# Optimization experiments

Measured on AMD Instinct MI355X. Metric: run time of the kernel, lower is better.

## Reference

```python
import jax, jax.numpy as jnp
import numpy as np

B, N = 512, 128          # molecules, max atoms
T = 10                   # NLSQ gradient-descent steps
STEP_EPS = 0.1
ALPHA, ALPHA_BASE = 5.0, 0.1
K_RANK, POWER_STEPS = 3, 10


def setup_inputs() -> dict:
    key = jax.random.key(0)
    k1, k2, k3, k4 = jax.random.split(key, 4)
    edge_pred = jax.random.normal(k1, (B, N, N, 2), dtype=jnp.float32)
    a = jax.random.randint(k2, (B, N, N), 0, 2)
    adj = ((a + a.transpose(0, 2, 1)) > 0).astype(jnp.int32)
    adj = adj * (1 - jnp.eye(N, dtype=jnp.int32))[None]  # symmetric, zero diagonal
    d_init = jnp.full((1,), 4.0, dtype=jnp.float32)      # learned scalar param
    u_init = jax.random.normal(k3, (B, N, 3), dtype=jnp.float32)   # power-iter inits (k=3 cols)
    x_noise = jax.random.normal(k4, (B, N, 3), dtype=jnp.float32)  # x_init additive noise
    return {"edge_pred": edge_pred, "adj": adj, "d_init": d_init,
            "u_init": u_init, "x_noise": x_noise}


def distances(X):
    # X: [B,N,3] -> [B,N,N]
    diff = X[:, None, :, :] - X[:, :, None, :]
    return jnp.sqrt(jnp.sum(diff * diff, axis=-1) + 0.01)


def distance_to_gram(D, mask):
    N_mol = jnp.sum(mask, axis=1)[:, 0].reshape(-1, 1, 1)
    D2 = D * D
    D_row = jnp.sum(D2, axis=1, keepdims=True) / N_mol
    D_col = jnp.sum(D2, axis=2, keepdims=True) / N_mol
    D_mean = jnp.sum(D2, axis=(1, 2), keepdims=True) / (N_mol * N_mol)
    return mask * (-0.5) * (D2 - D_row - D_col + D_mean)


def low_rank_approx_power(A, u_init):
    # A: [B,N,N]; u_init: [B,N,K_RANK] -> X: [B,N,K_RANK]
    A_lr = A
    cols = []
    for kx in range(K_RANK):
        u = u_init[..., kx:kx + 1]  # [B,N,1]
        for _ in range(POWER_STEPS):
            norm = jnp.sqrt(jnp.sum(u * u, axis=1, keepdims=True))
            u = u / jnp.maximum(norm, 1e-3)  # F.normalize(dim=1, eps=1e-3)
            u = jnp.matmul(A_lr, u)
        eig_sq = jnp.sum(u * u, axis=1, keepdims=True)
        u = u / jnp.power(eig_sq + 0.01, 0.25)
        cols.append(u)
        A_lr = A_lr - jnp.matmul(u, u.transpose(0, 2, 1))
    return jnp.concatenate(cols, axis=2)


def dist_nlsq(D, W, mask, u_init, x_noise):
    def objective(X):
        D_X = distances(X)
        U = jnp.sum(mask * W * jnp.square(D - D_X), axis=(1, 2)) / jnp.sum(mask, axis=(1, 2))
        return jnp.sum(U)

    gradfun = jax.grad(objective)
    Bg = distance_to_gram(D, mask)
    x0 = low_rank_approx_power(Bg, u_init) + x_noise

    def step(x, t):
        g = gradfun(x)
        dx = -STEP_EPS * g
        speed = jnp.sqrt(jnp.sum(dx * dx, axis=2, keepdims=True) + 0.001)
        alpha_t = ALPHA_BASE + (ALPHA - ALPHA_BASE) * ((T - t) / T)
        scale = alpha_t * jnp.tanh(speed / alpha_t) / speed
        return x + dx * scale, None

    x, _ = jax.lax.scan(step, x0, jnp.arange(T, dtype=jnp.float32))
    return x


def reference(edge_pred, adj, d_init, u_init, x_noise):
    diag_mask = adj.astype(jnp.float32)                      # [B,N,N], zero diagonal
    ep = edge_pred + edge_pred.transpose(0, 2, 1, 3)         # symmetrize
    preds = jax.nn.softplus(d_init + ep) * diag_mask[..., None]
    D, W = preds[..., 0], preds[..., 1]
    eye = jnp.eye(N, dtype=bool)[None]
    mask = jnp.where(eye, 1.0, diag_mask)                    # diagonal set to 1
    X = dist_nlsq(D, W, mask, u_init, x_noise)               # [B,N,3]
    return diag_mask * distances(X)
```

## Files before the change

### kernel.cpp

```cpp
#include <hip/hip_runtime.h>
#include <hip/hip_fp16.h>
#include <math.h>

#define NN   128
#define PSTR 132
#define NTH  512

__device__ __forceinline__ float sp_softplus(float x) {
    float p = __builtin_amdgcn_exp2f(fabsf(x) * -1.44269504f);
    float l = __builtin_amdgcn_logf(1.0f + p);
    return fmaxf(x, 0.0f) + 0.69314718f * l;
}
__device__ __forceinline__ float rdlane(float v, int l) {
    return __int_as_float(__builtin_amdgcn_readlane(__float_as_int(v), l));
}
__device__ __forceinline__ float rcpf(float x)  { return __builtin_amdgcn_rcpf(x); }
__device__ __forceinline__ float rsqf(float x)  { return __builtin_amdgcn_rsqf(x); }

__global__ void __launch_bounds__(NTH, 2)
ts_gcn_kernel(const float* __restrict__ edge_pred,
              const int*   __restrict__ adj,
              const float* __restrict__ d_init,
              const float* __restrict__ u_init,
              const float* __restrict__ x_noise,
              float* __restrict__ out)
{
    __shared__ __align__(16) float pool[NN * PSTR];
    __shared__ unsigned maskb[512];
    __shared__ int s_cntM, s_cntN0;

    float* scrA = pool;
    float* scrB = pool + 512;
    float* scrC = pool + 1024;
    float* Xx   = pool + 1536;
    float* Xy   = pool + 1664;
    float* Xz   = pool + 1792;
    float* r_s  = pool + 1920;

    const int b    = blockIdx.x;
    const int t    = threadIdx.x;
    const int lane = t & 63;
    const int i    = t & 127;
    const int q    = t >> 7;
    const int jb   = q * 32;
    const int lsel = jb & 63;
    const int hi6  = (t >> 6) & 1;

    const float dini = d_init[0];
    if (t == 0) { s_cntM = 0; s_cntN0 = 0; }

    const int4* adj4 = (const int4*)(adj + (size_t)b * 16384);
    #pragma unroll 4
    for (int k = 0; k < 8; ++k) {
        int e4 = t + k * 512;
        int4 v = adj4[e4];
        int ii = e4 >> 5, jj = (e4 & 31) * 4;
        float* p = &pool[ii * PSTR + jj];
        p[0] = __int_as_float(v.x); p[1] = __int_as_float(v.y);
        p[2] = __int_as_float(v.z); p[3] = __int_as_float(v.w);
    }
    __syncthreads();
    unsigned mword = 0;
    #pragma unroll
    for (int k = 0; k < 32; ++k) {
        int j = jb + k;
        int a = __float_as_int(pool[i * PSTR + j]) | __float_as_int(pool[j * PSTR + i]);
        if (a != 0 && i != j) mword |= (1u << k);
    }
    maskb[i * 4 + q] = mword;
    int cm = __popc(mword);
    #pragma unroll
    for (int off = 32; off; off >>= 1) cm += __shfl_xor(cm, off);
    if (lane == 0) atomicAdd(&s_cntM, cm);
    if (i == 0)    atomicAdd(&s_cntN0, __popc(mword));
    __syncthreads();

    const float4* ep4 = (const float4*)(edge_pred + (size_t)b * 32768);
    #pragma unroll 4
    for (int k = 0; k < 16; ++k) {
        int e2 = t + k * 512;
        float4 v = ep4[e2];
        int ii = e2 >> 6, jj = (e2 & 63) * 2;
        *(float2*)&pool[ii * PSTR + jj] = make_float2(v.x, v.z);
    }
    __syncthreads();
    float    Dfull[32];
    unsigned DWh[32];
    #pragma unroll
    for (int k = 0; k < 32; ++k) {
        int j = jb + k;
        float s = pool[i * PSTR + j] + pool[j * PSTR + i];
        float d = ((mword >> k) & 1) ? sp_softplus(dini + s) : 0.f;
        Dfull[k] = d;
        DWh[k] = (unsigned)__half_as_ushort(__float2half_rn(d));
    }
    __syncthreads();

    float rp = 0.f;
    #pragma unroll
    for (int k = 0; k < 32; ++k) rp = fmaf(Dfull[k], Dfull[k], rp);
    scrA[t] = rp;
    __syncthreads();
    if (t < NN)
        r_s[t] = (scrA[t] + scrA[t + 128]) + (scrA[t + 256] + scrA[t + 384]);
    __syncthreads();
    float mt = r_s[lane] + r_s[lane + 64];
    #pragma unroll
    for (int off = 32; off; off >>= 1) mt += __shfl_xor(mt, off);

    const float Nmol  = (float)(1 + s_cntN0);
    const float Minv  = 1.0f / (float)(128 + s_cntM);
    const float invN  = 1.0f / Nmol;
    const float cmean = mt * invN * invN;

    const float ri = r_s[i];
    float Bg[32];
    #pragma unroll
    for (int k = 0; k < 32; ++k) {
        int j = jb + k;
        float dv = Dfull[k];
        float v  = -0.5f * (dv * dv - ri * invN - r_s[j] * invN + cmean);
        bool msk = ((mword >> k) & 1) || (i == j);
        Bg[k] = msk ? v : 0.f;
    }
    __syncthreads();

    #pragma unroll 4
    for (int k = 0; k < 16; ++k) {
        int e2 = t + k * 512;
        float4 v = ep4[e2];
        int ii = e2 >> 6, jj = (e2 & 63) * 2;
        *(float2*)&pool[ii * PSTR + jj] = make_float2(v.y, v.w);
    }
    __syncthreads();
    #pragma unroll
    for (int k = 0; k < 32; ++k) {
        int j = jb + k;
        float s = pool[i * PSTR + j] + pool[j * PSTR + i];
        float w = ((mword >> k) & 1) ? sp_softplus(dini + s) : 0.f;
        DWh[k] |= ((unsigned)__half_as_ushort(__float2half_rn(w))) << 16;
    }
    __syncthreads();

    const float* ub = u_init  + (size_t)b * 384;
    const float* xb = x_noise + (size_t)b * 384;

    #pragma unroll 1
    for (int kx = 0; kx < 3; ++kx) {
        float ulo = ub[lane * 3 + kx];
        float uhi = ub[(lane + 64) * 3 + kx];
        float* rd = scrA; float* wr = scrB;
        #pragma unroll 1
        for (int s = 0; s < 10; ++s) {
            if (s) {
                ulo = (rd[lane]      + rd[lane + 128]) + (rd[lane + 256] + rd[lane + 384]);
                uhi = (rd[lane + 64] + rd[lane + 192]) + (rd[lane + 320] + rd[lane + 448]);
            }
            float n2 = fmaf(ulo, ulo, uhi * uhi);
            #pragma unroll
            for (int off = 32; off; off >>= 1) n2 += __shfl_xor(n2, off);
            float inv = rcpf(fmaxf(sqrtf(n2), 0.001f));
            float usel = (q < 2) ? ulo : uhi;
            float a0 = 0.f, a1 = 0.f;
            #pragma unroll
            for (int k = 0; k < 16; ++k) {
                a0 = fmaf(Bg[k],      rdlane(usel, lsel + k),      a0);
                a1 = fmaf(Bg[k + 16], rdlane(usel, lsel + k + 16), a1);
            }
            wr[t] = (a0 + a1) * inv;
            __syncthreads();
            float* tmp = rd; rd = wr; wr = tmp;
        }
        float ulo2 = (rd[lane]      + rd[lane + 128]) + (rd[lane + 256] + rd[lane + 384]);
        float uhi2 = (rd[lane + 64] + rd[lane + 192]) + (rd[lane + 320] + rd[lane + 448]);
        float e2 = fmaf(ulo2, ulo2, uhi2 * uhi2);
        #pragma unroll
        for (int off = 32; off; off >>= 1) e2 += __shfl_xor(e2, off);
        float esc  = rsqf(sqrtf(e2 + 0.01f));
        float ufi  = (hi6 ? uhi2 : ulo2) * esc;
        float uscl = ((q < 2) ? ulo2 : uhi2) * esc;
        #pragma unroll
        for (int k = 0; k < 32; ++k)
            Bg[k] = fmaf(-ufi, rdlane(uscl, lsel + k), Bg[k]);
        if (t < NN) {
            float* Xc = (kx == 0) ? Xx : (kx == 1) ? Xy : Xz;
            Xc[t] = ufi + xb[t * 3 + kx];
        }
        __syncthreads();
    }

    const float stepc = 0.4f * Minv;
    #pragma unroll 1
    for (int st = 0; st < 10; ++st) {
        float xix = Xx[i], xiy = Xy[i], xiz = Xz[i];
        float gx = 0.f, gy = 0.f, gz = 0.f;
        #pragma unroll
        for (int g = 0; g < 8; ++g) {
            float4 vx = *(const float4*)&Xx[jb + 4 * g];
            float4 vy = *(const float4*)&Xy[jb + 4 * g];
            float4 vz = *(const float4*)&Xz[jb + 4 * g];
            #pragma unroll
            for (int c = 0; c < 4; ++c) {
                int k = 4 * g + c;
                unsigned pw = DWh[k];
                float Dk = __half2float(__ushort_as_half((unsigned short)(pw & 0xffffu)));
                float Wk = __half2float(__ushort_as_half((unsigned short)(pw >> 16)));
                float jx = (c == 0) ? vx.x : (c == 1) ? vx.y : (c == 2) ? vx.z : vx.w;
                float jy = (c == 0) ? vy.x : (c == 1) ? vy.y : (c == 2) ? vy.z : vy.w;
                float jz = (c == 0) ? vz.x : (c == 1) ? vz.y : (c == 2) ? vz.z : vz.w;
                float dx = xix - jx, dy = xiy - jy, dz = xiz - jz;
                float d2 = fmaf(dx, dx, fmaf(dy, dy, fmaf(dz, dz, 0.01f)));
                float rv = rcpf(sqrtf(d2));
                float c2 = fmaf(Dk * rv, Wk, -Wk);
                gx = fmaf(c2, dx, gx);
                gy = fmaf(c2, dy, gy);
                gz = fmaf(c2, dz, gz);
            }
        }
        scrA[t] = gx; scrB[t] = gy; scrC[t] = gz;
        __syncthreads();
        if (t < NN) {
            float sx = (scrA[t] + scrA[t + 128]) + (scrA[t + 256] + scrA[t + 384]);
            float sy = (scrB[t] + scrB[t + 128]) + (scrB[t + 256] + scrB[t + 384]);
            float sz = (scrC[t] + scrC[t + 128]) + (scrC[t + 256] + scrC[t + 384]);
            float dxv = sx * stepc, dyv = sy * stepc, dzv = sz * stepc;
            float spd = sqrtf(fmaf(dxv, dxv, fmaf(dyv, dyv, fmaf(dzv, dzv, 0.001f))));
            float alpha = 0.1f + 4.9f * (float)(10 - st) * 0.1f;
            float z  = fminf(spd * rcpf(alpha), 20.0f);
            float e  = __builtin_amdgcn_exp2f(z * 2.88539008f);
            float th = (e - 1.0f) * rcpf(e + 1.0f);
            float scl = alpha * th * rcpf(spd);
            Xx[t] = fmaf(dxv, scl, Xx[t]);
            Xy[t] = fmaf(dyv, scl, Xy[t]);
            Xz[t] = fmaf(dzv, scl, Xz[t]);
        }
        __syncthreads();
    }

    float* ob = out + (size_t)b * 16384;
    #pragma unroll
    for (int k = 0; k < 8; ++k) {
        int e4 = t + k * 512;
        int ii = e4 >> 5, jjb = (e4 & 31) * 4;
        float xix = Xx[ii], xiy = Xy[ii], xiz = Xz[ii];
        float4 vx = *(const float4*)&Xx[jjb];
        float4 vy = *(const float4*)&Xy[jjb];
        float4 vz = *(const float4*)&Xz[jjb];
        unsigned mw = maskb[ii * 4 + (jjb >> 5)];
        float4 o;
        {
            float dx = xix - vx.x, dy = xiy - vy.x, dz = xiz - vz.x;
            float d2 = fmaf(dx, dx, fmaf(dy, dy, fmaf(dz, dz, 0.01f)));
            o.x = ((mw >> ((jjb + 0) & 31)) & 1) ? sqrtf(d2) : 0.f;
        }
        {
            float dx = xix - vx.y, dy = xiy - vy.y, dz = xiz - vz.y;
            float d2 = fmaf(dx, dx, fmaf(dy, dy, fmaf(dz, dz, 0.01f)));
            o.y = ((mw >> ((jjb + 1) & 31)) & 1) ? sqrtf(d2) : 0.f;
        }
        {
            float dx = xix - vx.z, dy = xiy - vy.z, dz = xiz - vz.z;
            float d2 = fmaf(dx, dx, fmaf(dy, dy, fmaf(dz, dz, 0.01f)));
            o.z = ((mw >> ((jjb + 2) & 31)) & 1) ? sqrtf(d2) : 0.f;
        }
        {
            float dx = xix - vx.w, dy = xiy - vy.w, dz = xiz - vz.w;
            float d2 = fmaf(dx, dx, fmaf(dy, dy, fmaf(dz, dz, 0.01f)));
            o.w = ((mw >> ((jjb + 3) & 31)) & 1) ? sqrtf(d2) : 0.f;
        }
        ((float4*)ob)[e4] = o;
    }
}

extern "C" void kernel_launch(void* const* d_in, const int* in_sizes, int n_in,
                              void* d_out, int out_size, void* d_ws, size_t ws_size,
                              hipStream_t stream) {
    const float* edge_pred = (const float*)d_in[0];
    const int*   adj       = (const int*)  d_in[1];
    const float* dinit     = (const float*)d_in[2];
    const float* u_init    = (const float*)d_in[3];
    const float* x_noise   = (const float*)d_in[4];
    float*       out       = (float*)d_out;

    ts_gcn_kernel<<<512, NTH, 0, stream>>>(edge_pred, adj, dinit, u_init, x_noise, out);
}
```

Before: 281.4 us.

## Process two molecules per block to share barriers and add ILP

Each block now handles two batch elements with duplicated register arrays and LDS pools, and the grid is halved. The goal is to interleave independent work from both molecules within each wave, hiding latency and amortizing the synchronization barriers. In exchange, register and LDS usage per block roughly doubles, and launch bounds drop to one block per CU, which can lower occupancy or cause spills.

```diff
diff --git a/kernel.cpp b/kernel.cpp
--- a/kernel.cpp
+++ b/kernel.cpp
@@ -17,7 +17,7 @@
 __device__ __forceinline__ float rcpf(float x)  { return __builtin_amdgcn_rcpf(x); }
 __device__ __forceinline__ float rsqf(float x)  { return __builtin_amdgcn_rsqf(x); }
 
-__global__ void __launch_bounds__(NTH, 2)
+__global__ void __launch_bounds__(NTH, 1)
 ts_gcn_kernel(const float* __restrict__ edge_pred,
               const int*   __restrict__ adj,
               const float* __restrict__ d_init,
@@ -25,19 +25,21 @@
               const float* __restrict__ x_noise,
               float* __restrict__ out)
 {
-    __shared__ __align__(16) float pool[NN * PSTR];
-    __shared__ unsigned maskb[512];
-    __shared__ int s_cntM, s_cntN0;
-
-    float* scrA = pool;
-    float* scrB = pool + 512;
-    float* scrC = pool + 1024;
-    float* Xx   = pool + 1536;
-    float* Xy   = pool + 1664;
-    float* Xz   = pool + 1792;
-    float* r_s  = pool + 1920;
-
-    const int b    = blockIdx.x;
+    __shared__ __align__(16) float poolA[NN * PSTR];
+    __shared__ __align__(16) float poolB[NN * PSTR];
+    __shared__ unsigned maskbA[512], maskbB[512];
+    __shared__ int cMA, cN0A, cMB, cN0B;
+
+    float* scr0A = poolA;          float* scr0B = poolB;
+    float* scr1A = poolA + 512;    float* scr1B = poolB + 512;
+    float* scr2A = poolA + 1024;   float* scr2B = poolB + 1024;
+    float* XxA   = poolA + 1536;   float* XxB   = poolB + 1536;
+    float* XyA   = poolA + 1664;   float* XyB   = poolB + 1664;
+    float* XzA   = poolA + 1792;   float* XzB   = poolB + 1792;
+    float* rsA   = poolA + 1920;   float* rsB   = poolB + 1920;
+
+    const int bA   = blockIdx.x * 2;
+    const int bB   = bA + 1;
     const int t    = threadIdx.x;
     const int lane = t & 63;
     const int i    = t & 127;
@@ -47,228 +49,332 @@
     const int hi6  = (t >> 6) & 1;
 
     const float dini = d_init[0];
-    if (t == 0) { s_cntM = 0; s_cntN0 = 0; }
-
-    const int4* adj4 = (const int4*)(adj + (size_t)b * 16384);
-    #pragma unroll 4
+    if (t == 0) { cMA = 0; cN0A = 0; cMB = 0; cN0B = 0; }
+
+    const int4* adjA4 = (const int4*)(adj + (size_t)bA * 16384);
+    const int4* adjB4 = (const int4*)(adj + (size_t)bB * 16384);
+    #pragma unroll 2
     for (int k = 0; k < 8; ++k) {
         int e4 = t + k * 512;
-        int4 v = adj4[e4];
+        int4 vA = adjA4[e4];
+        int4 vB = adjB4[e4];
         int ii = e4 >> 5, jj = (e4 & 31) * 4;
-        float* p = &pool[ii * PSTR + jj];
-        p[0] = __int_as_float(v.x); p[1] = __int_as_float(v.y);
-        p[2] = __int_as_float(v.z); p[3] = __int_as_float(v.w);
-    }
-    __syncthreads();
-    unsigned mword = 0;
+        float* pA = &poolA[ii * PSTR + jj];
+        float* pB = &poolB[ii * PSTR + jj];
+        pA[0] = __int_as_float(vA.x); pA[1] = __int_as_float(vA.y);
+        pA[2] = __int_as_float(vA.z); pA[3] = __int_as_float(vA.w);
+        pB[0] = __int_as_float(vB.x); pB[1] = __int_as_float(vB.y);
+        pB[2] = __int_as_float(vB.z); pB[3] = __int_as_float(vB.w);
+    }
+    __syncthreads();
+    unsigned mwA = 0, mwB = 0;
     #pragma unroll
     for (int k = 0; k < 32; ++k) {
         int j = jb + k;
-        int a = __float_as_int(pool[i * PSTR + j]) | __float_as_int(pool[j * PSTR + i]);
-        if (a != 0 && i != j) mword |= (1u << k);
-    }
-    maskb[i * 4 + q] = mword;
-    int cm = __popc(mword);
-    #pragma unroll
-    for (int off = 32; off; off >>= 1) cm += __shfl_xor(cm, off);
-    if (lane == 0) atomicAdd(&s_cntM, cm);
-    if (i == 0)    atomicAdd(&s_cntN0, __popc(mword));
-    __syncthreads();
-
-    const float4* ep4 = (const float4*)(edge_pred + (size_t)b * 32768);
-    #pragma unroll 4
+        int aA = __float_as_int(poolA[i * PSTR + j]) | __float_as_int(poolA[j * PSTR + i]);
+        int aB = __float_as_int(poolB[i * PSTR + j]) | __float_as_int(poolB[j * PSTR + i]);
+        if (aA != 0 && i != j) mwA |= (1u << k);
+        if (aB != 0 && i != j) mwB |= (1u << k);
+    }
+    maskbA[i * 4 + q] = mwA;
+    maskbB[i * 4 + q] = mwB;
+    int cmA = __popc(mwA), cmB = __popc(mwB);
+    #pragma unroll
+    for (int off = 32; off; off >>= 1) { cmA += __shfl_xor(cmA, off); cmB += __shfl_xor(cmB, off); }
+    if (lane == 0) { atomicAdd(&cMA, cmA); atomicAdd(&cMB, cmB); }
+    if (i == 0)    { atomicAdd(&cN0A, __popc(mwA)); atomicAdd(&cN0B, __popc(mwB)); }
+    __syncthreads();
+
+    const float4* epA4 = (const float4*)(edge_pred + (size_t)bA * 32768);
+    const float4* epB4 = (const float4*)(edge_pred + (size_t)bB * 32768);
+    #pragma unroll 2
     for (int k = 0; k < 16; ++k) {
         int e2 = t + k * 512;
-        float4 v = ep4[e2];
+        float4 vA = epA4[e2];
+        float4 vB = epB4[e2];
         int ii = e2 >> 6, jj = (e2 & 63) * 2;
-        *(float2*)&pool[ii * PSTR + jj] = make_float2(v.x, v.z);
-    }
-    __syncthreads();
-    float    Dfull[32];
-    unsigned DWh[32];
+        *(float2*)&poolA[ii * PSTR + jj] = make_float2(vA.x, vA.z);
+        *(float2*)&poolB[ii * PSTR + jj] = make_float2(vB.x, vB.z);
+    }
+    __syncthreads();
+    float    DfA[32], DfB[32];
+    unsigned DWhA[32], DWhB[32];
     #pragma unroll
     for (int k = 0; k < 32; ++k) {
         int j = jb + k;
-        float s = pool[i * PSTR + j] + pool[j * PSTR + i];
-        float d = ((mword >> k) & 1) ? sp_softplus(dini + s) : 0.f;
-        Dfull[k] = d;
-        DWh[k] = (unsigned)__half_as_ushort(__float2half_rn(d));
-    }
-    __syncthreads();
-
-    float rp = 0.f;
-    #pragma unroll
-    for (int k = 0; k < 32; ++k) rp = fmaf(Dfull[k], Dfull[k], rp);
-    scrA[t] = rp;
-    __syncthreads();
-    if (t < NN)
-        r_s[t] = (scrA[t] + scrA[t + 128]) + (scrA[t + 256] + scrA[t + 384]);
-    __syncthreads();
-    float mt = r_s[lane] + r_s[lane + 64];
-    #pragma unroll
-    for (int off = 32; off; off >>= 1) mt += __shfl_xor(mt, off);
-
-    const float Nmol  = (float)(1 + s_cntN0);
-    const float Minv  = 1.0f / (float)(128 + s_cntM);
-    const float invN  = 1.0f / Nmol;
-    const float cmean = mt * invN * invN;
-
-    const float ri = r_s[i];
-    float Bg[32];
+        float sA = poolA[i * PSTR + j] + poolA[j * PSTR + i];
+        float sB = poolB[i * PSTR + j] + poolB[j * PSTR + i];
+        float dA = ((mwA >> k) & 1) ? sp_softplus(dini + sA) : 0.f;
+        float dB = ((mwB >> k) & 1) ? sp_softplus(dini + sB) : 0.f;
+        DfA[k] = dA; DWhA[k] = (unsigned)__half_as_ushort(__float2half_rn(dA));
+        DfB[k] = dB; DWhB[k] = (unsigned)__half_as_ushort(__float2half_rn(dB));
+    }
+    __syncthreads();
+
+    float rpA = 0.f, rpB = 0.f;
+    #pragma unroll
+    for (int k = 0; k < 32; ++k) { rpA = fmaf(DfA[k], DfA[k], rpA); rpB = fmaf(DfB[k], DfB[k], rpB); }
+    scr0A[t] = rpA; scr0B[t] = rpB;
+    __syncthreads();
+    if (t < NN) {
+        rsA[t] = (scr0A[t] + scr0A[t + 128]) + (scr0A[t + 256] + scr0A[t + 384]);
+    } else if (t < 256) {
+        int tt = t - 128;
+        rsB[tt] = (scr0B[tt] + scr0B[tt + 128]) + (scr0B[tt + 256] + scr0B[tt + 384]);
+    }
+    __syncthreads();
+    float mtA = rsA[lane] + rsA[lane + 64];
+    float mtB = rsB[lane] + rsB[lane + 64];
+    #pragma unroll
+    for (int off = 32; off; off >>= 1) { mtA += __shfl_xor(mtA, off); mtB += __shfl_xor(mtB, off); }
+
+    const float invNA  = 1.0f / (float)(1 + cN0A);
+    const float invNB  = 1.0f / (float)(1 + cN0B);
+    const float MinvA  = 1.0f / (float)(128 + cMA);
+    const float MinvB  = 1.0f / (float)(128 + cMB);
+    const float cmeanA = mtA * invNA * invNA;
+    const float cmeanB = mtB * invNB * invNB;
+
+    const float riA = rsA[i], riB = rsB[i];
+    float BgA[32], BgB[32];
     #pragma unroll
     for (int k = 0; k < 32; ++k) {
         int j = jb + k;
-        float dv = Dfull[k];
-        float v  = -0.5f * (dv * dv - ri * invN - r_s[j] * invN + cmean);
-        bool msk = ((mword >> k) & 1) || (i == j);
-        Bg[k] = msk ? v : 0.f;
-    }
-    __syncthreads();
-
-    #pragma unroll 4
+        float dA = DfA[k];
+        float vA = -0.5f * (dA * dA - riA * invNA - rsA[j] * invNA + cmeanA);
+        BgA[k] = (((mwA >> k) & 1) || (i == j)) ? vA : 0.f;
+        float dB = DfB[k];
+        float vB = -0.5f * (dB * dB - riB * invNB - rsB[j] * invNB + cmeanB);
+        BgB[k] = (((mwB >> k) & 1) || (i == j)) ? vB : 0.f;
+    }
+    __syncthreads();
+
+    #pragma unroll 2
     for (int k = 0; k < 16; ++k) {
         int e2 = t + k * 512;
-        float4 v = ep4[e2];
+        float4 vA = epA4[e2];
+        float4 vB = epB4[e2];
         int ii = e2 >> 6, jj = (e2 & 63) * 2;
-        *(float2*)&pool[ii * PSTR + jj] = make_float2(v.y, v.w);
+        *(float2*)&poolA[ii * PSTR + jj] = make_float2(vA.y, vA.w);
+        *(float2*)&poolB[ii * PSTR + jj] = make_float2(vB.y, vB.w);
     }
     __syncthreads();
     #pragma unroll
     for (int k = 0; k < 32; ++k) {
         int j = jb + k;
-        float s = pool[i * PSTR + j] + pool[j * PSTR + i];
-        float w = ((mword >> k) & 1) ? sp_softplus(dini + s) : 0.f;
-        DWh[k] |= ((unsigned)__half_as_ushort(__float2half_rn(w))) << 16;
-    }
-    __syncthreads();
-
-    const float* ub = u_init  + (size_t)b * 384;
-    const float* xb = x_noise + (size_t)b * 384;
+        float sA = poolA[i * PSTR + j] + poolA[j * PSTR + i];
+        float sB = poolB[i * PSTR + j] + poolB[j * PSTR + i];
+        float wA = ((mwA >> k) & 1) ? sp_softplus(dini + sA) : 0.f;
+        float wB = ((mwB >> k) & 1) ? sp_softplus(dini + sB) : 0.f;
+        DWhA[k] |= ((unsigned)__half_as_ushort(__float2half_rn(wA))) << 16;
+        DWhB[k] |= ((unsigned)__half_as_ushort(__float2half_rn(wB))) << 16;
+    }
+    __syncthreads();
+
+    const float* ubA = u_init  + (size_t)bA * 384;
+    const float* ubB = u_init  + (size_t)bB * 384;
+    const float* xbA = x_noise + (size_t)bA * 384;
+    const float* xbB = x_noise + (size_t)bB * 384;
 
     #pragma unroll 1
     for (int kx = 0; kx < 3; ++kx) {
-        float ulo = ub[lane * 3 + kx];
-        float uhi = ub[(lane + 64) * 3 + kx];
-        float* rd = scrA; float* wr = scrB;
+        float uloA = ubA[lane * 3 + kx], uhiA = ubA[(lane + 64) * 3 + kx];
+        float uloB = ubB[lane * 3 + kx], uhiB = ubB[(lane + 64) * 3 + kx];
+        float* rdA = scr0A; float* wrA = scr1A;
+        float* rdB = scr0B; float* wrB = scr1B;
         #pragma unroll 1
         for (int s = 0; s < 10; ++s) {
             if (s) {
-                ulo = (rd[lane]      + rd[lane + 128]) + (rd[lane + 256] + rd[lane + 384]);
-                uhi = (rd[lane + 64] + rd[lane + 192]) + (rd[lane + 320] + rd[lane + 448]);
+                uloA = (rdA[lane]      + rdA[lane + 128]) + (rdA[lane + 256] + rdA[lane + 384]);
+                uhiA = (rdA[lane + 64] + rdA[lane + 192]) + (rdA[lane + 320] + rdA[lane + 448]);
+                uloB = (rdB[lane]      + rdB[lane + 128]) + (rdB[lane + 256] + rdB[lane + 384]);
+                uhiB = (rdB[lane + 64] + rdB[lane + 192]) + (rdB[lane + 320] + rdB[lane + 448]);
             }
-            float n2 = fmaf(ulo, ulo, uhi * uhi);
+            float n2A = fmaf(uloA, uloA, uhiA * uhiA);
+            float n2B = fmaf(uloB, uloB, uhiB * uhiB);
             #pragma unroll
-            for (int off = 32; off; off >>= 1) n2 += __shfl_xor(n2, off);
-            float inv = rcpf(fmaxf(sqrtf(n2), 0.001f));
-            float usel = (q < 2) ? ulo : uhi;
-            float a0 = 0.f, a1 = 0.f;
+            for (int off = 32; off; off >>= 1) { n2A += __shfl_xor(n2A, off); n2B += __shfl_xor(n2B, off); }
+            float invA = rcpf(fmaxf(sqrtf(n2A), 0.001f));
+            float invB = rcpf(fmaxf(sqrtf(n2B), 0.001f));
+            float uselA = (q < 2) ? uloA : uhiA;
+            float uselB = (q < 2) ? uloB : uhiB;
+            float a0A = 0.f, a1A = 0.f, a0B = 0.f, a1B = 0.f;
             #pragma unroll
             for (int k = 0; k < 16; ++k) {
-                a0 = fmaf(Bg[k],      rdlane(usel, lsel + k),      a0);
-                a1 = fmaf(Bg[k + 16], rdlane(usel, lsel + k + 16), a1);
+                a0A = fmaf(BgA[k],      rdlane(uselA, lsel + k),      a0A);
+                a1A = fmaf(BgA[k + 16], rdlane(uselA, lsel + k + 16), a1A);
+                a0B = fmaf(BgB[k],      rdlane(uselB, lsel + k),      a0B);
+                a1B = fmaf(BgB[k + 16], rdlane(uselB, lsel + k + 16), a1B);
             }
-            wr[t] = (a0 + a1) * inv;
+            wrA[t] = (a0A + a1A) * invA;
+            wrB[t] = (a0B + a1B) * invB;
             __syncthreads();
-            float* tmp = rd; rd = wr; wr = tmp;
-        }
-        float ulo2 = (rd[lane]      + rd[lane + 128]) + (rd[lane + 256] + rd[lane + 384]);
-        float uhi2 = (rd[lane + 64] + rd[lane + 192]) + (rd[lane + 320] + rd[lane + 448]);
-        float e2 = fmaf(ulo2, ulo2, uhi2 * uhi2);
+            float* tp;
+            tp = rdA; rdA = wrA; wrA = tp;
+            tp = rdB; rdB = wrB; wrB = tp;
+        }
+        float ulo2A = (rdA[lane]      + rdA[lane + 128]) + (rdA[lane + 256] + rdA[lane + 384]);
+        float uhi2A = (rdA[lane + 64] + rdA[lane + 192]) + (rdA[lane + 320] + rdA[lane + 448]);
+        float ulo2B = (rdB[lane]      + rdB[lane + 128]) + (rdB[lane + 256] + rdB[lane + 384]);
+        float uhi2B = (rdB[lane + 64] + rdB[lane + 192]) + (rdB[lane + 320] + rdB[lane + 448]);
+        float e2A = fmaf(ulo2A, ulo2A, uhi2A * uhi2A);
+        float e2B = fmaf(ulo2B, ulo2B, uhi2B * uhi2B);
         #pragma unroll
-        for (int off = 32; off; off >>= 1) e2 += __shfl_xor(e2, off);
-        float esc  = rsqf(sqrtf(e2 + 0.01f));
-        float ufi  = (hi6 ? uhi2 : ulo2) * esc;
-        float uscl = ((q < 2) ? ulo2 : uhi2) * esc;
+        for (int off = 32; off; off >>= 1) { e2A += __shfl_xor(e2A, off); e2B += __shfl_xor(e2B, off); }
+        float escA = rsqf(sqrtf(e2A + 0.01f));
+        float escB = rsqf(sqrtf(e2B + 0.01f));
+        float ufiA  = (hi6 ? uhi2A : ulo2A) * escA;
+        float ufiB  = (hi6 ? uhi2B : ulo2B) * escB;
+        float usclA = ((q < 2) ? ulo2A : uhi2A) * escA;
+        float usclB = ((q < 2) ? ulo2B : uhi2B) * escB;
         #pragma unroll
-        for (int k = 0; k < 32; ++k)
-            Bg[k] = fmaf(-ufi, rdlane(uscl, lsel + k), Bg[k]);
+        for (int k = 0; k < 32; ++k) {
+            BgA[k] = fmaf(-ufiA, rdlane(usclA, lsel + k), BgA[k]);
+            BgB[k] = fmaf(-ufiB, rdlane(usclB, lsel + k), BgB[k]);
+        }
         if (t < NN) {
-            float* Xc = (kx == 0) ? Xx : (kx == 1) ? Xy : Xz;
-            Xc[t] = ufi + xb[t * 3 + kx];
+            float* Xc = (kx == 0) ? XxA : (kx == 1) ? XyA : XzA;
+            Xc[t] = ufiA + xbA[t * 3 + kx];
+        } else if (t < 256) {
+            int tt = t - 128;
+            float* Xc = (kx == 0) ? XxB : (kx == 1) ? XyB : XzB;
+            Xc[tt] = ufiB + xbB[tt * 3 + kx];
         }
         __syncthreads();
     }
 
-    const float stepc = 0.4f * Minv;
+    const float stepcA = 0.4f * MinvA;
+    const float stepcB = 0.4f * MinvB;
     #pragma unroll 1
     for (int st = 0; st < 10; ++st) {
-        float xix = Xx[i], xiy = Xy[i], xiz = Xz[i];
-        float gx = 0.f, gy = 0.f, gz = 0.f;
+        float xixA = XxA[i], xiyA = XyA[i], xizA = XzA[i];
+        float xixB = XxB[i], xiyB = XyB[i], xizB = XzB[i];
+        float gxA = 0.f, gyA = 0.f, gzA = 0.f;
+        float gxB = 0.f, gyB = 0.f, gzB = 0.f;
         #pragma unroll
         for (int g = 0; g < 8; ++g) {
-            float4 vx = *(const float4*)&Xx[jb + 4 * g];
-            float4 vy = *(const float4*)&Xy[jb + 4 * g];
-            float4 vz = *(const float4*)&Xz[jb + 4 * g];
+            float4 vxA = *(const float4*)&XxA[jb + 4 * g];
+            float4 vyA = *(const float4*)&XyA[jb + 4 * g];
+            float4 vzA = *(const float4*)&XzA[jb + 4 * g];
+            float4 vxB = *(const float4*)&XxB[jb + 4 * g];
+            float4 vyB = *(const float4*)&XyB[jb + 4 * g];
+            float4 vzB = *(const float4*)&XzB[jb + 4 * g];
             #pragma unroll
             for (int c = 0; c < 4; ++c) {
                 int k = 4 * g + c;
-                unsigned pw = DWh[k];
-                float Dk = __half2float(__ushort_as_half((unsigned short)(pw & 0xffffu)));
-                float Wk = __half2float(__ushort_as_half((unsigned short)(pw >> 16)));
-                float jx = (c == 0) ? vx.x : (c == 1) ? vx.y : (c == 2) ? vx.z : vx.w;
-                float jy = (c == 0) ? vy.x : (c == 1) ? vy.y : (c == 2) ? vy.z : vy.w;
-                float jz = (c == 0) ? vz.x : (c == 1) ? vz.y : (c == 2) ? vz.z : vz.w;
-                float dx = xix - jx, dy = xiy - jy, dz = xiz - jz;
-                float d2 = fmaf(dx, dx, fmaf(dy, dy, fmaf(dz, dz, 0.01f)));
-                float rv = rcpf(sqrtf(d2));
-                float c2 = fmaf(Dk * rv, Wk, -Wk);
-                gx = fmaf(c2, dx, gx);
-                gy = fmaf(c2, dy, gy);
-                gz = fmaf(c2, dz, gz);
+                {
+                    unsigned pw = DWhA[k];
+                    float Dk = __half2float(__ushort_as_half((unsigned short)(pw & 0xffffu)));
+                    float Wk = __half2float(__ushort_as_half((unsigned short)(pw >> 16)));
+                    float jx = (c == 0) ? vxA.x : (c == 1) ? vxA.y : (c == 2) ? vxA.z : vxA.w;
+                    float jy = (c == 0) ? vyA.x : (c == 1) ? vyA.y : (c == 2) ? vyA.z : vyA.w;
+                    float jz = (c == 0) ? vzA.x : (c == 1) ? vzA.y : (c == 2) ? vzA.z : vzA.w;
+                    float dx = xixA - jx, dy = xiyA - jy, dz = xizA - jz;
+                    float d2 = fmaf(dx, dx, fmaf(dy, dy, fmaf(dz, dz, 0.01f)));
+                    float rv = rcpf(sqrtf(d2));
+                    float c2 = fmaf(Dk * rv, Wk, -Wk);
+                    gxA = fmaf(c2, dx, gxA); gyA = fmaf(c2, dy, gyA); gzA = fmaf(c2, dz, gzA);
+                }
+                {
+                    unsigned pw = DWhB[k];
+                    float Dk = __half2float(__ushort_as_half((unsigned short)(pw & 0xffffu)));
+                    float Wk = __half2float(__ushort_as_half((unsigned short)(pw >> 16)));
+                    float jx = (c == 0) ? vxB.x : (c == 1) ? vxB.y : (c == 2) ? vxB.z : vxB.w;
+                    float jy = (c == 0) ? vyB.x : (c == 1) ? vyB.y : (c == 2) ? vyB.z : vyB.w;
+                    float jz = (c == 0) ? vzB.x : (c == 1) ? vzB.y : (c == 2) ? vzB.z : vzB.w;
+                    float dx = xixB - jx, dy = xiyB - jy, dz = xizB - jz;
+                    float d2 = fmaf(dx, dx, fmaf(dy, dy, fmaf(dz, dz, 0.01f)));
+                    float rv = rcpf(sqrtf(d2));
+                    float c2 = fmaf(Dk * rv, Wk, -Wk);
+                    gxB = fmaf(c2, dx, gxB); gyB = fmaf(c2, dy, gyB); gzB = fmaf(c2, dz, gzB);
+                }
             }
         }
-        scrA[t] = gx; scrB[t] = gy; scrC[t] = gz;
+        scr0A[t] = gxA; scr1A[t] = gyA; scr2A[t] = gzA;
+        scr0B[t] = gxB; scr1B[t] = gyB; scr2B[t] = gzB;
         __syncthreads();
+        float alpha = 0.1f + 4.9f * (float)(10 - st) * 0.1f;
         if (t < NN) {
-            float sx = (scrA[t] + scrA[t + 128]) + (scrA[t + 256] + scrA[t + 384]);
-            float sy = (scrB[t] + scrB[t + 128]) + (scrB[t + 256] + scrB[t + 384]);
-            float sz = (scrC[t] + scrC[t + 128]) + (scrC[t + 256] + scrC[t + 384]);
-            float dxv = sx * stepc, dyv = sy * stepc, dzv = sz * stepc;
+            float sx = (scr0A[t] + scr0A[t + 128]) + (scr0A[t + 256] + scr0A[t + 384]);
+            float sy = (scr1A[t] + scr1A[t + 128]) + (scr1A[t + 256] + scr1A[t + 384]);
+            float sz = (scr2A[t] + scr2A[t + 128]) + (scr2A[t + 256] + scr2A[t + 384]);
+            float dxv = sx * stepcA, dyv = sy * stepcA, dzv = sz * stepcA;
             float spd = sqrtf(fmaf(dxv, dxv, fmaf(dyv, dyv, fmaf(dzv, dzv, 0.001f))));
-            float alpha = 0.1f + 4.9f * (float)(10 - st) * 0.1f;
             float z  = fminf(spd * rcpf(alpha), 20.0f);
             float e  = __builtin_amdgcn_exp2f(z * 2.88539008f);
             float th = (e - 1.0f) * rcpf(e + 1.0f);
             float scl = alpha * th * rcpf(spd);
-            Xx[t] = fmaf(dxv, scl, Xx[t]);
-            Xy[t] = fmaf(dyv, scl, Xy[t]);
-            Xz[t] = fmaf(dzv, scl, Xz[t]);
+            XxA[t] = fmaf(dxv, scl, XxA[t]);
+            XyA[t] = fmaf(dyv, scl, XyA[t]);
+            XzA[t] = fmaf(dzv, scl, XzA[t]);
+        } else if (t < 256) {
+            int tt = t - 128;
+            float sx = (scr0B[tt] + scr0B[tt + 128]) + (scr0B[tt + 256] + scr0B[tt + 384]);
+            float sy = (scr1B[tt] + scr1B[tt + 128]) + (scr1B[tt + 256] + scr1B[tt + 384]);
+            float sz = (scr2B[tt] + scr2B[tt + 128]) + (scr2B[tt + 256] + scr2B[tt + 384]);
+            float dxv = sx * stepcB, dyv = sy * stepcB, dzv = sz * stepcB;
+            float spd = sqrtf(fmaf(dxv, dxv, fmaf(dyv, dyv, fmaf(dzv, dzv, 0.001f))));
+            float z  = fminf(spd * rcpf(alpha), 20.0f);
+            float e  = __builtin_amdgcn_exp2f(z * 2.88539008f);
+            float th = (e - 1.0f) * rcpf(e + 1.0f);
+            float scl = alpha * th * rcpf(spd);
+            XxB[tt] = fmaf(dxv, scl, XxB[tt]);
+            XyB[tt] = fmaf(dyv, scl, XyB[tt]);
+            XzB[tt] = fmaf(dzv, scl, XzB[tt]);
         }
         __syncthreads();
     }
 
-    float* ob = out + (size_t)b * 16384;
-    #pragma unroll
+    float* obA = out + (size_t)bA * 16384;
+    float* obB = out + (size_t)bB * 16384;
+    #pragma unroll 2
     for (int k = 0; k < 8; ++k) {
         int e4 = t + k * 512;
         int ii = e4 >> 5, jjb = (e4 & 31) * 4;
-        float xix = Xx[ii], xiy = Xy[ii], xiz = Xz[ii];
-        float4 vx = *(const float4*)&Xx[jjb];
-        float4 vy = *(const float4*)&Xy[jjb];
-        float4 vz = *(const float4*)&Xz[jjb];
-        unsigned mw = maskb[ii * 4 + (jjb >> 5)];
-        float4 o;
         {
-            float dx = xix - vx.x, dy = xiy - vy.x, dz = xiz - vz.x;
-            float d2 = fmaf(dx, dx, fmaf(dy, dy, fmaf(dz, dz, 0.01f)));
+            float xix = XxA[ii], xiy = XyA[ii], xiz = XzA[ii];
+            float4 vx = *(const float4*)&XxA[jjb];
+            float4 vy = *(const float4*)&XyA[jjb];
+            float4 vz = *(const float4*)&XzA[jjb];
+            unsigned mw = maskbA[ii * 4 + (jjb >> 5)];
+            float4 o;
+            float dx, dy, dz, d2;
+            dx = xix - vx.x; dy = xiy - vy.x; dz = xiz - vz.x;
+            d2 = fmaf(dx, dx, fmaf(dy, dy, fmaf(dz, dz, 0.01f)));
             o.x = ((mw >> ((jjb + 0) & 31)) & 1) ? sqrtf(d2) : 0.f;
+            dx = xix - vx.y; dy = xiy - vy.y; dz = xiz - vz.y;
+            d2 = fmaf(dx, dx, fmaf(dy, dy, fmaf(dz, dz, 0.01f)));
+            o.y = ((mw >> ((jjb + 1) & 31)) & 1) ? sqrtf(d2) : 0.f;
+            dx = xix - vx.z; dy = xiy - vy.z; dz = xiz - vz.z;
+            d2 = fmaf(dx, dx, fmaf(dy, dy, fmaf(dz, dz, 0.01f)));
+            o.z = ((mw >> ((jjb + 2) & 31)) & 1) ? sqrtf(d2) : 0.f;
+            dx = xix - vx.w; dy = xiy - vy.w; dz = xiz - vz.w;
+            d2 = fmaf(dx, dx, fmaf(dy, dy, fmaf(dz, dz, 0.01f)));
+            o.w = ((mw >> ((jjb + 3) & 31)) & 1) ? sqrtf(d2) : 0.f;
+            ((float4*)obA)[e4] = o;
         }
         {
-            float dx = xix - vx.y, dy = xiy - vy.y, dz = xiz - vz.y;
-            float d2 = fmaf(dx, dx, fmaf(dy, dy, fmaf(dz, dz, 0.01f)));
+            float xix = XxB[ii], xiy = XyB[ii], xiz = XzB[ii];
+            float4 vx = *(const float4*)&XxB[jjb];
+            float4 vy = *(const float4*)&XyB[jjb];
+            float4 vz = *(const float4*)&XzB[jjb];
+            unsigned mw = maskbB[ii * 4 + (jjb >> 5)];
+            float4 o;
+            float dx, dy, dz, d2;
+            dx = xix - vx.x; dy = xiy - vy.x; dz = xiz - vz.x;
+            d2 = fmaf(dx, dx, fmaf(dy, dy, fmaf(dz, dz, 0.01f)));
+            o.x = ((mw >> ((jjb + 0) & 31)) & 1) ? sqrtf(d2) : 0.f;
+            dx = xix - vx.y; dy = xiy - vy.y; dz = xiz - vz.y;
+            d2 = fmaf(dx, dx, fmaf(dy, dy, fmaf(dz, dz, 0.01f)));
             o.y = ((mw >> ((jjb + 1) & 31)) & 1) ? sqrtf(d2) : 0.f;
-        }
-        {
-            float dx = xix - vx.z, dy = xiy - vy.z, dz = xiz - vz.z;
-            float d2 = fmaf(dx, dx, fmaf(dy, dy, fmaf(dz, dz, 0.01f)));
+            dx = xix - vx.z; dy = xiy - vy.z; dz = xiz - vz.z;
+            d2 = fmaf(dx, dx, fmaf(dy, dy, fmaf(dz, dz, 0.01f)));
             o.z = ((mw >> ((jjb + 2) & 31)) & 1) ? sqrtf(d2) : 0.f;
-        }
-        {
-            float dx = xix - vx.w, dy = xiy - vy.w, dz = xiz - vz.w;
-            float d2 = fmaf(dx, dx, fmaf(dy, dy, fmaf(dz, dz, 0.01f)));
+            dx = xix - vx.w; dy = xiy - vy.w; dz = xiz - vz.w;
+            d2 = fmaf(dx, dx, fmaf(dy, dy, fmaf(dz, dz, 0.01f)));
             o.w = ((mw >> ((jjb + 3) & 31)) & 1) ? sqrtf(d2) : 0.f;
-        }
-        ((float4*)ob)[e4] = o;
+            ((float4*)obB)[e4] = o;
+        }
     }
 }
 
@@ -282,5 +388,5 @@
     const float* x_noise   = (const float*)d_in[4];
     float*       out       = (float*)d_out;
 
-    ts_gcn_kernel<<<512, NTH, 0, stream>>>(edge_pred, adj, dinit, u_init, x_noise, out);
+    ts_gcn_kernel<<<256, NTH, 0, stream>>>(edge_pred, adj, dinit, u_init, x_noise, out);
 }
```

Result: slower. 322.4 us (+14.6%).

## Halve block to 256 threads, each thread covering 64 columns per row

Applied to the files above, without the earlier changes.

Changes the per-molecule decomposition from 512 threads with 32 columns each to 256 threads with 64 columns each. Register arrays (D/W packed, Bg) double, and the cross-thread reductions through shared memory shrink from four partials to two. The intent is less synchronization and reduction overhead per block and more register-resident work per thread. In exchange, register pressure rises sharply (about 128+ live values) and could cause spills or cap occupancy, which the waves_per_eu attribute tries to control.

```diff
diff --git a/kernel.cpp b/kernel.cpp
--- a/kernel.cpp
+++ b/kernel.cpp
@@ -4,7 +4,7 @@
 
 #define NN   128
 #define PSTR 132
-#define NTH  512
+#define NTH  256
 
 __device__ __forceinline__ float sp_softplus(float x) {
     float p = __builtin_amdgcn_exp2f(fabsf(x) * -1.44269504f);
@@ -17,7 +17,7 @@
 __device__ __forceinline__ float rcpf(float x)  { return __builtin_amdgcn_rcpf(x); }
 __device__ __forceinline__ float rsqf(float x)  { return __builtin_amdgcn_rsqf(x); }
 
-__global__ void __launch_bounds__(NTH, 2)
+__global__ void __launch_bounds__(NTH) __attribute__((amdgpu_waves_per_eu(2, 2)))
 ts_gcn_kernel(const float* __restrict__ edge_pred,
               const int*   __restrict__ adj,
               const float* __restrict__ d_init,
@@ -30,20 +30,19 @@
     __shared__ int s_cntM, s_cntN0;
 
     float* scrA = pool;
-    float* scrB = pool + 512;
-    float* scrC = pool + 1024;
-    float* Xx   = pool + 1536;
-    float* Xy   = pool + 1664;
-    float* Xz   = pool + 1792;
-    float* r_s  = pool + 1920;
+    float* scrB = pool + 256;
+    float* scrC = pool + 512;
+    float* Xx   = pool + 768;
+    float* Xy   = pool + 896;
+    float* Xz   = pool + 1024;
+    float* r_s  = pool + 1152;
 
     const int b    = blockIdx.x;
     const int t    = threadIdx.x;
     const int lane = t & 63;
     const int i    = t & 127;
     const int q    = t >> 7;
-    const int jb   = q * 32;
-    const int lsel = jb & 63;
+    const int jb   = q * 64;
     const int hi6  = (t >> 6) & 1;
 
     const float dini = d_init[0];
@@ -51,8 +50,8 @@
 
     const int4* adj4 = (const int4*)(adj + (size_t)b * 16384);
     #pragma unroll 4
-    for (int k = 0; k < 8; ++k) {
-        int e4 = t + k * 512;
+    for (int k = 0; k < 16; ++k) {
+        int e4 = t + k * 256;
         int4 v = adj4[e4];
         int ii = e4 >> 5, jj = (e4 & 31) * 4;
         float* p = &pool[ii * PSTR + jj];
@@ -60,37 +59,38 @@
         p[2] = __int_as_float(v.z); p[3] = __int_as_float(v.w);
     }
     __syncthreads();
-    unsigned mword = 0;
-    #pragma unroll
-    for (int k = 0; k < 32; ++k) {
+    unsigned long long mw = 0;
+    #pragma unroll
+    for (int k = 0; k < 64; ++k) {
         int j = jb + k;
         int a = __float_as_int(pool[i * PSTR + j]) | __float_as_int(pool[j * PSTR + i]);
-        if (a != 0 && i != j) mword |= (1u << k);
-    }
-    maskb[i * 4 + q] = mword;
-    int cm = __popc(mword);
+        if (a != 0 && i != j) mw |= (1ull << k);
+    }
+    maskb[i * 4 + q * 2]     = (unsigned)mw;
+    maskb[i * 4 + q * 2 + 1] = (unsigned)(mw >> 32);
+    int cm = __popcll(mw);
     #pragma unroll
     for (int off = 32; off; off >>= 1) cm += __shfl_xor(cm, off);
     if (lane == 0) atomicAdd(&s_cntM, cm);
-    if (i == 0)    atomicAdd(&s_cntN0, __popc(mword));
+    if (i == 0)    atomicAdd(&s_cntN0, __popcll(mw));
     __syncthreads();
 
     const float4* ep4 = (const float4*)(edge_pred + (size_t)b * 32768);
     #pragma unroll 4
-    for (int k = 0; k < 16; ++k) {
-        int e2 = t + k * 512;
+    for (int k = 0; k < 32; ++k) {
+        int e2 = t + k * 256;
         float4 v = ep4[e2];
         int ii = e2 >> 6, jj = (e2 & 63) * 2;
         *(float2*)&pool[ii * PSTR + jj] = make_float2(v.x, v.z);
     }
     __syncthreads();
-    float    Dfull[32];
-    unsigned DWh[32];
-    #pragma unroll
-    for (int k = 0; k < 32; ++k) {
+    float    Dfull[64];
+    unsigned DWh[64];
+    #pragma unroll
+    for (int k = 0; k < 64; ++k) {
         int j = jb + k;
         float s = pool[i * PSTR + j] + pool[j * PSTR + i];
-        float d = ((mword >> k) & 1) ? sp_softplus(dini + s) : 0.f;
+        float d = ((mw >> k) & 1) ? sp_softplus(dini + s) : 0.f;
         Dfull[k] = d;
         DWh[k] = (unsigned)__half_as_ushort(__float2half_rn(d));
     }
@@ -98,11 +98,10 @@
 
     float rp = 0.f;
     #pragma unroll
-    for (int k = 0; k < 32; ++k) rp = fmaf(Dfull[k], Dfull[k], rp);
+    for (int k = 0; k < 64; ++k) rp = fmaf(Dfull[k], Dfull[k], rp);
     scrA[t] = rp;
     __syncthreads();
-    if (t < NN)
-        r_s[t] = (scrA[t] + scrA[t + 128]) + (scrA[t + 256] + scrA[t + 384]);
+    if (t < NN) r_s[t] = scrA[t] + scrA[t + 128];
     __syncthreads();
     float mt = r_s[lane] + r_s[lane + 64];
     #pragma unroll
@@ -114,30 +113,30 @@
     const float cmean = mt * invN * invN;
 
     const float ri = r_s[i];
-    float Bg[32];
-    #pragma unroll
-    for (int k = 0; k < 32; ++k) {
+    float Bg[64];
+    #pragma unroll
+    for (int k = 0; k < 64; ++k) {
         int j = jb + k;
         float dv = Dfull[k];
         float v  = -0.5f * (dv * dv - ri * invN - r_s[j] * invN + cmean);
-        bool msk = ((mword >> k) & 1) || (i == j);
+        bool msk = ((mw >> k) & 1) || (i == j);
         Bg[k] = msk ? v : 0.f;
     }
     __syncthreads();
 
     #pragma unroll 4
-    for (int k = 0; k < 16; ++k) {
-        int e2 = t + k * 512;
+    for (int k = 0; k < 32; ++k) {
+        int e2 = t + k * 256;
         float4 v = ep4[e2];
         int ii = e2 >> 6, jj = (e2 & 63) * 2;
         *(float2*)&pool[ii * PSTR + jj] = make_float2(v.y, v.w);
     }
     __syncthreads();
     #pragma unroll
-    for (int k = 0; k < 32; ++k) {
+    for (int k = 0; k < 64; ++k) {
         int j = jb + k;
         float s = pool[i * PSTR + j] + pool[j * PSTR + i];
-        float w = ((mword >> k) & 1) ? sp_softplus(dini + s) : 0.f;
+        float w = ((mw >> k) & 1) ? sp_softplus(dini + s) : 0.f;
         DWh[k] |= ((unsigned)__half_as_ushort(__float2half_rn(w))) << 16;
     }
     __syncthreads();
@@ -153,35 +152,35 @@
         #pragma unroll 1
         for (int s = 0; s < 10; ++s) {
             if (s) {
-                ulo = (rd[lane]      + rd[lane + 128]) + (rd[lane + 256] + rd[lane + 384]);
-                uhi = (rd[lane + 64] + rd[lane + 192]) + (rd[lane + 320] + rd[lane + 448]);
+                ulo = rd[lane]      + rd[lane + 128];
+                uhi = rd[lane + 64] + rd[lane + 192];
             }
             float n2 = fmaf(ulo, ulo, uhi * uhi);
             #pragma unroll
             for (int off = 32; off; off >>= 1) n2 += __shfl_xor(n2, off);
             float inv = rcpf(fmaxf(sqrtf(n2), 0.001f));
-            float usel = (q < 2) ? ulo : uhi;
+            float usel = q ? uhi : ulo;
             float a0 = 0.f, a1 = 0.f;
             #pragma unroll
-            for (int k = 0; k < 16; ++k) {
-                a0 = fmaf(Bg[k],      rdlane(usel, lsel + k),      a0);
-                a1 = fmaf(Bg[k + 16], rdlane(usel, lsel + k + 16), a1);
+            for (int k = 0; k < 32; ++k) {
+                a0 = fmaf(Bg[k],      rdlane(usel, k),      a0);
+                a1 = fmaf(Bg[k + 32], rdlane(usel, k + 32), a1);
             }
             wr[t] = (a0 + a1) * inv;
             __syncthreads();
             float* tmp = rd; rd = wr; wr = tmp;
         }
-        float ulo2 = (rd[lane]      + rd[lane + 128]) + (rd[lane + 256] + rd[lane + 384]);
-        float uhi2 = (rd[lane + 64] + rd[lane + 192]) + (rd[lane + 320] + rd[lane + 448]);
+        float ulo2 = rd[lane]      + rd[lane + 128];
+        float uhi2 = rd[lane + 64] + rd[lane + 192];
         float e2 = fmaf(ulo2, ulo2, uhi2 * uhi2);
         #pragma unroll
         for (int off = 32; off; off >>= 1) e2 += __shfl_xor(e2, off);
         float esc  = rsqf(sqrtf(e2 + 0.01f));
         float ufi  = (hi6 ? uhi2 : ulo2) * esc;
-        float uscl = ((q < 2) ? ulo2 : uhi2) * esc;
+        float uscl = (q ? uhi2 : ulo2) * esc;
         #pragma unroll
-        for (int k = 0; k < 32; ++k)
-            Bg[k] = fmaf(-ufi, rdlane(uscl, lsel + k), Bg[k]);
+        for (int k = 0; k < 64; ++k)
+            Bg[k] = fmaf(-ufi, rdlane(uscl, k), Bg[k]);
         if (t < NN) {
             float* Xc = (kx == 0) ? Xx : (kx == 1) ? Xy : Xz;
             Xc[t] = ufi + xb[t * 3 + kx];
@@ -195,7 +194,7 @@
         float xix = Xx[i], xiy = Xy[i], xiz = Xz[i];
         float gx = 0.f, gy = 0.f, gz = 0.f;
         #pragma unroll
-        for (int g = 0; g < 8; ++g) {
+        for (int g = 0; g < 16; ++g) {
             float4 vx = *(const float4*)&Xx[jb + 4 * g];
             float4 vy = *(const float4*)&Xy[jb + 4 * g];
             float4 vz = *(const float4*)&Xz[jb + 4 * g];
@@ -220,9 +219,9 @@
         scrA[t] = gx; scrB[t] = gy; scrC[t] = gz;
         __syncthreads();
         if (t < NN) {
-            float sx = (scrA[t] + scrA[t + 128]) + (scrA[t + 256] + scrA[t + 384]);
-            float sy = (scrB[t] + scrB[t + 128]) + (scrB[t + 256] + scrB[t + 384]);
-            float sz = (scrC[t] + scrC[t + 128]) + (scrC[t + 256] + scrC[t + 384]);
+            float sx = scrA[t] + scrA[t + 128];
+            float sy = scrB[t] + scrB[t + 128];
+            float sz = scrC[t] + scrC[t + 128];
             float dxv = sx * stepc, dyv = sy * stepc, dzv = sz * stepc;
             float spd = sqrtf(fmaf(dxv, dxv, fmaf(dyv, dyv, fmaf(dzv, dzv, 0.001f))));
             float alpha = 0.1f + 4.9f * (float)(10 - st) * 0.1f;
@@ -238,36 +237,29 @@
     }
 
     float* ob = out + (size_t)b * 16384;
-    #pragma unroll
-    for (int k = 0; k < 8; ++k) {
-        int e4 = t + k * 512;
+    #pragma unroll 4
+    for (int k = 0; k < 16; ++k) {
+        int e4 = t + k * 256;
         int ii = e4 >> 5, jjb = (e4 & 31) * 4;
         float xix = Xx[ii], xiy = Xy[ii], xiz = Xz[ii];
         float4 vx = *(const float4*)&Xx[jjb];
         float4 vy = *(const float4*)&Xy[jjb];
         float4 vz = *(const float4*)&Xz[jjb];
-        unsigned mw = maskb[ii * 4 + (jjb >> 5)];
+        unsigned mwo = maskb[ii * 4 + (jjb >> 5)];
         float4 o;
-        {
-            float dx = xix - vx.x, dy = xiy - vy.x, dz = xiz - vz.x;
-            float d2 = fmaf(dx, dx, fmaf(dy, dy, fmaf(dz, dz, 0.01f)));
-            o.x = ((mw >> ((jjb + 0) & 31)) & 1) ? sqrtf(d2) : 0.f;
-        }
-        {
-            float dx = xix - vx.y, dy = xiy - vy.y, dz = xiz - vz.y;
-            float d2 = fmaf(dx, dx, fmaf(dy, dy, fmaf(dz, dz, 0.01f)));
-            o.y = ((mw >> ((jjb + 1) & 31)) & 1) ? sqrtf(d2) : 0.f;
-        }
-        {
-            float dx = xix - vx.z, dy = xiy - vy.z, dz = xiz - vz.z;
-            float d2 = fmaf(dx, dx, fmaf(dy, dy, fmaf(dz, dz, 0.01f)));
-            o.z = ((mw >> ((jjb + 2) & 31)) & 1) ? sqrtf(d2) : 0.f;
-        }
-        {
-            float dx = xix - vx.w, dy = xiy - vy.w, dz = xiz - vz.w;
-            float d2 = fmaf(dx, dx, fmaf(dy, dy, fmaf(dz, dz, 0.01f)));
-            o.w = ((mw >> ((jjb + 3) & 31)) & 1) ? sqrtf(d2) : 0.f;
-        }
+        float dx, dy, dz, d2;
+        dx = xix - vx.x; dy = xiy - vy.x; dz = xiz - vz.x;
+        d2 = fmaf(dx, dx, fmaf(dy, dy, fmaf(dz, dz, 0.01f)));
+        o.x = ((mwo >> ((jjb + 0) & 31)) & 1) ? sqrtf(d2) : 0.f;
+        dx = xix - vx.y; dy = xiy - vy.y; dz = xiz - vz.y;
+        d2 = fmaf(dx, dx, fmaf(dy, dy, fmaf(dz, dz, 0.01f)));
+        o.y = ((mwo >> ((jjb + 1) & 31)) & 1) ? sqrtf(d2) : 0.f;
+        dx = xix - vx.z; dy = xiy - vy.z; dz = xiz - vz.z;
+        d2 = fmaf(dx, dx, fmaf(dy, dy, fmaf(dz, dz, 0.01f)));
+        o.z = ((mwo >> ((jjb + 2) & 31)) & 1) ? sqrtf(d2) : 0.f;
+        dx = xix - vx.w; dy = xiy - vy.w; dz = xiz - vz.w;
+        d2 = fmaf(dx, dx, fmaf(dy, dy, fmaf(dz, dz, 0.01f)));
+        o.w = ((mwo >> ((jjb + 3) & 31)) & 1) ? sqrtf(d2) : 0.f;
         ((float4*)ob)[e4] = o;
     }
 }
```

Measured after the change: 318.0 us. 13.0% more time.
